# Performance work log

Measured on AMD Instinct MI355X. Metric: run time of the kernel, lower is better.

The kernel has to match this reference:

```python
import jax, jax.numpy as jnp
import numpy as np

B, N, D, H, IN, HID = 16, 1024, 256, 8, 256, 1024
HD = IN // H  # head dim = 32
EPS = 1e-5


def layer_norm(x, g, b):
    mu = jnp.mean(x, axis=-1, keepdims=True)
    var = jnp.var(x, axis=-1, keepdims=True)
    return (x - mu) / jnp.sqrt(var + EPS) * g + b


def setup_inputs() -> dict:
    key = jax.random.key(0)
    ks = jax.random.split(key, 12)
    s = 0.02
    return {
        "x": jax.random.normal(ks[0], (B, N, D), jnp.float32),
        "coords": jax.random.normal(ks[1], (B, N, 2), jnp.float32),
        "g1": jnp.ones((D,), jnp.float32),
        "b1": jnp.zeros((D,), jnp.float32),
        "Wqkv": jax.random.normal(ks[2], (3 * IN, D), jnp.float32) * s,
        "Wproj": jax.random.normal(ks[3], (IN, IN), jnp.float32) * s,
        "bproj": jnp.zeros((IN,), jnp.float32),
        "g2": jnp.ones((D,), jnp.float32),
        "b2": jnp.zeros((D,), jnp.float32),
        "W1": jax.random.normal(ks[4], (HID, D), jnp.float32) * s,
        "bb1": jnp.zeros((HID,), jnp.float32),
        "W2": jax.random.normal(ks[5], (D, HID), jnp.float32) * s,
        "bb2": jnp.zeros((D,), jnp.float32),
    }


def reference(x, coords, g1, b1, Wqkv, Wproj, bproj, g2, b2, W1, bb1, W2, bb2):
    # ---- Attention branch (pre-norm) ----
    h = layer_norm(x, g1, b1)                       # [B,N,D]
    qkv = h @ Wqkv.T                                # [B,N,3*IN]
    qkv = qkv.reshape(B, N, 3, H, HD).transpose(2, 0, 3, 1, 4)  # [3,B,H,N,HD]
    q, k, v = qkv[0], qkv[1], qkv[2]
    scale = HD ** -0.5
    attn = jnp.einsum('bhid,bhjd->bhij', q * scale, k)  # [B,H,N,N]
    attn = jax.nn.softmax(attn, axis=-1)
    o = jnp.einsum('bhij,bhjd->bhid', attn, v)      # [B,H,N,HD]
    o = o.transpose(0, 2, 1, 3).reshape(B, N, IN)   # [B,N,IN]
    o = o @ Wproj.T + bproj
    o = o + h                                       # residual inside Attention (vs normed input)
    x = x + o                                       # Block residual (double residual, faithful)
    # ---- MLP branch ----
    h2 = layer_norm(x, g2, b2)
    m = jax.nn.gelu(h2 @ W1.T + bb1, approximate=False) @ W2.T + bb2
    return x + m
```

## Files before the change

kernel.cpp:

```cpp
#include <hip/hip_runtime.h>
#include <hip/hip_bf16.h>
#include <math.h>

#define Bdim 16
#define Ndim 1024
#define Ddim 256
#define Hdim 8
#define HDdim 32
#define INdim 256
#define HIDdim 1024
#define Tdim (Bdim * Ndim)

typedef __attribute__((ext_vector_type(8)))  short bf16x8;
typedef __attribute__((ext_vector_type(4)))  short bf16x4;
typedef __attribute__((ext_vector_type(16))) float f32x16;
typedef unsigned int u32;

__device__ inline short f2bf(float x) {
    union { __hip_bfloat16 b; short s; } u;
    u.b = __float2bfloat16(x);
    return u.s;
}

__device__ inline float bf2f(short s) {
    return __uint_as_float(((u32)(unsigned short)s) << 16);
}

__device__ inline float fexp2(float x) {
#if __has_builtin(__builtin_amdgcn_exp2f)
    return __builtin_amdgcn_exp2f(x);
#else
    return exp2f(x);
#endif
}

__device__ inline u32 pack2bf(float a, float b) {
#if __has_builtin(__builtin_amdgcn_cvt_pk_bf16_f32)
    typedef __attribute__((ext_vector_type(2))) __bf16 bf16x2_t;
    union { bf16x2_t v; u32 u; } c;
    c.v = __builtin_amdgcn_cvt_pk_bf16_f32(a, b);
    return c.u;
#else
    u32 ua = __float_as_uint(a), ub = __float_as_uint(b);
    return ((ua + 0x8000u) >> 16) | ((ub + 0x8000u) & 0xffff0000u);
#endif
}

__device__ inline void plswap(u32 &a, u32 &b) {
    asm volatile("v_permlane32_swap_b32 %0, %1" : "+v"(a), "+v"(b));
}

__device__ inline float gelu_exact(float v) {
    return 0.5f * v * (1.0f + erff(v * 0.70710678118654752f));
}

#define N4_QKV  (3 * INdim * Ddim / 4)
#define N4_PROJ (INdim * INdim / 4)
#define N4_W1   (HIDdim * Ddim / 4)
#define N4_W2   (Ddim * HIDdim / 4)

__global__ __launch_bounds__(256) void cvt_all_kernel(const float* __restrict__ s0,
                                                      const float* __restrict__ s1,
                                                      const float* __restrict__ s2,
                                                      const float* __restrict__ s3,
                                                      short* __restrict__ d0,
                                                      short* __restrict__ d1,
                                                      short* __restrict__ d2,
                                                      short* __restrict__ d3) {
    int i = blockIdx.x * 256 + threadIdx.x;
    const float* src; short* dst; int j;
    if (i < N4_QKV)                          { src = s0; dst = d0; j = i; }
    else if (i < N4_QKV + N4_PROJ)           { src = s1; dst = d1; j = i - N4_QKV; }
    else if (i < N4_QKV + N4_PROJ + N4_W1)   { src = s2; dst = d2; j = i - N4_QKV - N4_PROJ; }
    else                                     { src = s3; dst = d3; j = i - N4_QKV - N4_PROJ - N4_W1; }
    float4 v = ((const float4*)src)[j];
    bf16x4 b;
    b[0] = f2bf(v.x); b[1] = f2bf(v.y); b[2] = f2bf(v.z); b[3] = f2bf(v.w);
    ((bf16x4*)dst)[j] = b;
}

__global__ __launch_bounds__(256) void ln4_kernel(const float* __restrict__ x,
                                                  const float* __restrict__ g,
                                                  const float* __restrict__ b,
                                                  float* __restrict__ outf,
                                                  short* __restrict__ outb) {
    int w = threadIdx.x >> 6, lane = threadIdx.x & 63;
    int row = blockIdx.x * 4 + w;
    float4 v = ((const float4*)x)[(size_t)row * 64 + lane];
    float s  = (v.x + v.y) + (v.z + v.w);
    float s2 = (v.x * v.x + v.y * v.y) + (v.z * v.z + v.w * v.w);
    #pragma unroll
    for (int off = 32; off; off >>= 1) {
        s  += __shfl_xor(s,  off, 64);
        s2 += __shfl_xor(s2, off, 64);
    }
    float mu   = s * (1.0f / Ddim);
    float var  = s2 * (1.0f / Ddim) - mu * mu;
    float rstd = rsqrtf(var + 1e-5f);
    float4 gg = ((const float4*)g)[lane];
    float4 bb = ((const float4*)b)[lane];
    float4 r;
    r.x = (v.x - mu) * rstd * gg.x + bb.x;
    r.y = (v.y - mu) * rstd * gg.y + bb.y;
    r.z = (v.z - mu) * rstd * gg.z + bb.z;
    r.w = (v.w - mu) * rstd * gg.w + bb.w;
    if (outf) ((float4*)outf)[(size_t)row * 64 + lane] = r;
    bf16x4 rb;
    rb[0] = f2bf(r.x); rb[1] = f2bf(r.y); rb[2] = f2bf(r.z); rb[3] = f2bf(r.w);
    ((bf16x4*)outb)[(size_t)row * 64 + lane] = rb;
}

#define EPI_NONE 0
#define EPI_PROJ 1
#define EPI_GELU 2
#define EPI_RES  3
#define EPI_QKV  4

#define GPAD32 40
#define SCALE2Q 0.25505654249892417f

template <int EPI, int BN>
__global__ __launch_bounds__(256) void gemm_mfma(const short* __restrict__ A,
                                                 const short* __restrict__ W,
                                                 void* __restrict__ Cv,
                                                 int M, int N, int K,
                                                 const float* __restrict__ bias,
                                                 const float* __restrict__ add1,
                                                 const float* __restrict__ add2) {
    __shared__ short As[64 * GPAD32];
    __shared__ short Bs[BN * GPAD32];
    const int tid = threadIdx.x, w = tid >> 6, lane = tid & 63;
    const int col = lane & 31;
    const int half_id = lane >> 5;

    const int nbx = gridDim.x;
    const int flat = blockIdx.y * nbx + blockIdx.x;
    const int cpx = (nbx * (int)gridDim.y) >> 3;
    const int swz = (flat & 7) * cpx + (flat >> 3);
    const int m0 = (swz / nbx) * 64, n0 = (swz % nbx) * BN;

    const int wm = (w & 1) * 32;
    const int wn = (BN == 128) ? (w >> 1) * 64 : (w >> 1) * 32;
    constexpr int TN = (BN == 128) ? 2 : 1;

    f32x16 acc[TN];
    #pragma unroll
    for (int t = 0; t < TN; ++t) acc[t] = 0.0f;

    const int sra = tid >> 2, ssa = (tid & 3) * 8;
    const int srb = (BN == 128) ? (tid >> 1) : (tid >> 2);
    const int ssb = (BN == 128) ? (tid & 1) * 16 : (tid & 3) * 8;
    constexpr int NB = (BN == 128) ? 2 : 1;

    const short* pAsrc = &A[(size_t)(m0 + sra) * K + ssa];
    const short* pBsrc = &W[(size_t)(n0 + srb) * K + ssb];

    bf16x8 pa, pb[NB];
    pa = *(const bf16x8*)&pAsrc[0];
    #pragma unroll
    for (int j = 0; j < NB; ++j) pb[j] = *(const bf16x8*)&pBsrc[j * 8];

    const int T = K >> 5;
    for (int kt = 0; kt < T; ++kt) {
        __syncthreads();
        *(bf16x8*)&As[sra * GPAD32 + ssa] = pa;
        #pragma unroll
        for (int j = 0; j < NB; ++j) *(bf16x8*)&Bs[srb * GPAD32 + ssb + j * 8] = pb[j];
        __syncthreads();

        if (kt + 1 < T) {
            const short* a = pAsrc + (kt + 1) * 32;
            const short* b = pBsrc + (kt + 1) * 32;
            pa = *(const bf16x8*)&a[0];
            #pragma unroll
            for (int j = 0; j < NB; ++j) pb[j] = *(const bf16x8*)&b[j * 8];
        }

        #pragma unroll
        for (int ks = 0; ks < 2; ++ks) {
            bf16x8 af = *(const bf16x8*)&As[(wm + col) * GPAD32 + ks * 16 + half_id * 8];
            bf16x8 bfv[TN];
            #pragma unroll
            for (int t = 0; t < TN; ++t)
                bfv[t] = *(const bf16x8*)&Bs[(wn + t * 32 + col) * GPAD32 + ks * 16 + half_id * 8];
            #pragma unroll
            for (int t = 0; t < TN; ++t)
                acc[t] = __builtin_amdgcn_mfma_f32_32x32x16_bf16(af, bfv[t], acc[t], 0, 0, 0);
        }
    }

    float* Cf = (float*)Cv;
    short* Cb = (short*)Cv;
    #pragma unroll
    for (int r = 0; r < 16; ++r) {
        int row = m0 + wm + (r & 3) + 8 * (r >> 2) + 4 * half_id;
        #pragma unroll
        for (int t = 0; t < TN; ++t) {
            int cn = n0 + wn + t * 32 + col;
            size_t off = (size_t)row * N + cn;
            float v = acc[t][r];
            if (EPI != EPI_NONE && EPI != EPI_QKV) v += bias[cn];
            if (EPI == EPI_QKV && cn < 256) v *= SCALE2Q;
            if (EPI == EPI_GELU) v = gelu_exact(v);
            if (EPI == EPI_PROJ) v += add1[off] + add2[off];
            if (EPI == EPI_RES)  v += add1[off];
            if (EPI == EPI_PROJ || EPI == EPI_RES) Cf[off] = v;
            else                                   Cb[off] = f2bf(v);
        }
    }
}

#define VTPAD 136

__global__ __launch_bounds__(256) void vtrans_kernel(const short* __restrict__ qkv,
                                                     short* __restrict__ vT) {
    __shared__ short Tl[32 * VTPAD];
    const int tid = threadIdx.x;
    const int bh = blockIdx.x, c = blockIdx.y;
    const int b = bh >> 3, head = bh & 7;
    {
        int r = tid >> 1, hv = tid & 1;
        const short* src = qkv + (size_t)b * Ndim * 768 + (size_t)(c * 128 + r) * 768
                           + 512 + head * 32 + hv * 16;
        bf16x8 v0 = *(const bf16x8*)&src[0];
        bf16x8 v1 = *(const bf16x8*)&src[8];
        #pragma unroll
        for (int i = 0; i < 8; ++i) {
            Tl[(hv * 16 + i) * VTPAD + r]     = v0[i];
            Tl[(hv * 16 + 8 + i) * VTPAD + r] = v1[i];
        }
    }
    __syncthreads();
    {
        int d = tid >> 3, j16 = (tid & 7) * 16;
        short* dst = vT + (size_t)(bh * 32 + d) * Ndim + c * 128 + j16;
        *(bf16x8*)&dst[0] = *(const bf16x8*)&Tl[d * VTPAD + j16];
        *(bf16x8*)&dst[8] = *(const bf16x8*)&Tl[d * VTPAD + j16 + 8];
    }
}

#define KVPAD 40
#define CHUNK 128

__global__ __launch_bounds__(256) void attn_mfma_kernel(const short* __restrict__ qkv,
                                                        const short* __restrict__ vT,
                                                        short* __restrict__ opart,
                                                        float* __restrict__ lpart) {
    __shared__ short Ks[CHUNK * KVPAD];
    __shared__ short Vt[32 * VTPAD];

    const int tid = threadIdx.x;
    const int w = tid >> 6;
    const int lane = tid & 63;
    const int col = lane & 31;
    const int half_id = lane >> 5;

    const int bh = blockIdx.y;
    const int b = bh >> 3, head = bh & 7;
    const int q0w = blockIdx.x * 128 + w * 32;
    const int part = blockIdx.z;

    const size_t qkvb = (size_t)b * Ndim * 768;
    short* op = opart + (size_t)part * Tdim * 256;
    float* lp = lpart + (size_t)part * Tdim * 8;

    const int sr = tid >> 1, shv = tid & 1;
    const short* ksrc = qkv + qkvb + (size_t)sr * 768 + 256 + head * 32 + shv * 16;
    const int sd = tid >> 3, sj16 = (tid & 7) * 16;
    const short* vsrc = vT + (size_t)(bh * 32 + sd) * Ndim + sj16;

    bf16x8 qf[2];
    {
        const short* qrow = qkv + qkvb + (size_t)(q0w + col) * 768 + head * 32;
        #pragma unroll
        for (int kh = 0; kh < 2; ++kh)
            qf[kh] = *(const bf16x8*)&qrow[kh * 16 + half_id * 8];
    }

    bf16x8 vone;
    #pragma unroll
    for (int i = 0; i < 8; ++i) vone[i] = (short)0x3F80;

    f32x16 o_acc = 0.0f, l_acc = 0.0f;

    const int c0 = part * 4;

    bf16x8 rk0, rk1, rv0, rv1;
    {
        const short* kp = ksrc + (size_t)(c0 * CHUNK) * 768;
        rk0 = *(const bf16x8*)&kp[0];
        rk1 = *(const bf16x8*)&kp[8];
        const short* vp = vsrc + c0 * CHUNK;
        rv0 = *(const bf16x8*)&vp[0];
        rv1 = *(const bf16x8*)&vp[8];
    }

    #pragma unroll
    for (int ci = 0; ci < 4; ++ci) {
        if (ci != 0) __syncthreads();
        *(bf16x8*)&Ks[sr * KVPAD + shv * 16]     = rk0;
        *(bf16x8*)&Ks[sr * KVPAD + shv * 16 + 8] = rk1;
        *(bf16x8*)&Vt[sd * VTPAD + sj16]     = rv0;
        *(bf16x8*)&Vt[sd * VTPAD + sj16 + 8] = rv1;
        __syncthreads();

        if (ci < 3) {
            const short* kp = ksrc + (size_t)((c0 + ci + 1) * CHUNK) * 768;
            rk0 = *(const bf16x8*)&kp[0];
            rk1 = *(const bf16x8*)&kp[8];
            const short* vp = vsrc + (c0 + ci + 1) * CHUNK;
            rv0 = *(const bf16x8*)&vp[0];
            rv1 = *(const bf16x8*)&vp[8];
        }

        f32x16 s_cur;
        {
            bf16x8 kf0 = *(bf16x8*)&Ks[col * KVPAD + half_id * 8];
            bf16x8 kf1 = *(bf16x8*)&Ks[col * KVPAD + 16 + half_id * 8];
            f32x16 z = 0.0f;
            z = __builtin_amdgcn_mfma_f32_32x32x16_bf16(kf0, qf[0], z, 0, 0, 0);
            z = __builtin_amdgcn_mfma_f32_32x32x16_bf16(kf1, qf[1], z, 0, 0, 0);
            s_cur = z;
        }
        #pragma unroll
        for (int jt = 0; jt < 4; ++jt) {
            f32x16 s_next;
            if (jt < 3) {
                bf16x8 kf0 = *(bf16x8*)&Ks[((jt + 1) * 32 + col) * KVPAD + half_id * 8];
                bf16x8 kf1 = *(bf16x8*)&Ks[((jt + 1) * 32 + col) * KVPAD + 16 + half_id * 8];
                f32x16 z = 0.0f;
                z = __builtin_amdgcn_mfma_f32_32x32x16_bf16(kf0, qf[0], z, 0, 0, 0);
                z = __builtin_amdgcn_mfma_f32_32x32x16_bf16(kf1, qf[1], z, 0, 0, 0);
                s_next = z;
            }

            bf16x8 vf0 = *(bf16x8*)&Vt[col * VTPAD + jt * 32 + half_id * 8];
            bf16x8 vf1 = *(bf16x8*)&Vt[col * VTPAD + jt * 32 + 16 + half_id * 8];

            u32 wd[8];
            #pragma unroll
            for (int g = 0; g < 8; ++g) {
                float e0 = fexp2(s_cur[2 * g + 0]);
                float e1 = fexp2(s_cur[2 * g + 1]);
                wd[g] = pack2bf(e0, e1);
            }
            plswap(wd[0], wd[2]); plswap(wd[1], wd[3]);
            plswap(wd[4], wd[6]); plswap(wd[5], wd[7]);

            union { u32 u[4]; bf16x8 v; } p0, p1;
            p0.u[0] = wd[0]; p0.u[1] = wd[1]; p0.u[2] = wd[2]; p0.u[3] = wd[3];
            p1.u[0] = wd[4]; p1.u[1] = wd[5]; p1.u[2] = wd[6]; p1.u[3] = wd[7];

            __builtin_amdgcn_s_setprio(1);
            o_acc = __builtin_amdgcn_mfma_f32_32x32x16_bf16(p0.v, vf0, o_acc, 0, 0, 0);
            o_acc = __builtin_amdgcn_mfma_f32_32x32x16_bf16(p1.v, vf1, o_acc, 0, 0, 0);
            l_acc = __builtin_amdgcn_mfma_f32_32x32x16_bf16(p0.v, vone, l_acc, 0, 0, 0);
            l_acc = __builtin_amdgcn_mfma_f32_32x32x16_bf16(p1.v, vone, l_acc, 0, 0, 0);
            __builtin_amdgcn_s_setprio(0);

            if (jt < 3) s_cur = s_next;
        }
    }

    #pragma unroll
    for (int r = 0; r < 16; ++r) {
        int q_r = (r & 3) + 8 * (r >> 2) + 4 * half_id;
        size_t gq = (size_t)(b * Ndim + q0w + q_r);
        op[gq * INdim + head * 32 + col] = f2bf(o_acc[r]);
    }
    if (col < 16) {
        int r = col;
        int q_r = (r & 3) + 8 * (r >> 2) + 4 * half_id;
        lp[(size_t)(b * Ndim + q0w + q_r) * 8 + head] = l_acc[r];
    }
}

__global__ __launch_bounds__(256) void combine_kernel(const short* __restrict__ opart,
                                                      const float* __restrict__ lpart,
                                                      short* __restrict__ oat) {
    int i = blockIdx.x * 256 + threadIdx.x;
    size_t base = (size_t)i * 8;
    int gq = (int)(base >> 8);
    int head = ((int)(base & 255)) >> 5;
    bf16x8 a = ((const bf16x8*)opart)[i];
    bf16x8 b = ((const bf16x8*)(opart + (size_t)Tdim * 256))[i];
    float l = lpart[(size_t)gq * 8 + head] + lpart[(size_t)Tdim * 8 + (size_t)gq * 8 + head];
    float rl = 1.0f / l;
    bf16x8 r;
    #pragma unroll
    for (int j = 0; j < 8; ++j) r[j] = f2bf((bf2f(a[j]) + bf2f(b[j])) * rl);
    ((bf16x8*)oat)[i] = r;
}

extern "C" void kernel_launch(void* const* d_in, const int* in_sizes, int n_in,
                              void* d_out, int out_size, void* d_ws, size_t ws_size,
                              hipStream_t stream) {
    const float* x     = (const float*)d_in[0];
    const float* g1    = (const float*)d_in[2];
    const float* b1    = (const float*)d_in[3];
    const float* Wqkv  = (const float*)d_in[4];
    const float* Wproj = (const float*)d_in[5];
    const float* bproj = (const float*)d_in[6];
    const float* g2    = (const float*)d_in[7];
    const float* b2    = (const float*)d_in[8];
    const float* W1    = (const float*)d_in[9];
    const float* bb1   = (const float*)d_in[10];
    const float* W2    = (const float*)d_in[11];
    const float* bb2   = (const float*)d_in[12];
    float* out = (float*)d_out;

    char* ws = (char*)d_ws;
    float* h      = (float*)(ws);
    short* h_bf   = (short*)(ws + (size_t)(16u << 20));
    short* qkv_bf = (short*)(ws + (size_t)(24u << 20));
    float* xnew   = (float*)(ws + (size_t)(24u << 20));
    short* oat_bf = (short*)(ws + (size_t)(40u << 20));
    short* opart  = (short*)(ws + (size_t)(48u << 20));
    short* mid_bf = (short*)(ws + (size_t)(48u << 20));
    float* lpart  = (float*)(ws + (size_t)(80u << 20));
    short* vT     = (short*)(ws + (size_t)(81u << 20));
    short* wqkv_b = (short*)(ws + (size_t)(89u << 20));
    short* wproj_b= (short*)(ws + (size_t)(89u << 20) + 768 * 1024);
    short* w1_b   = (short*)(ws + (size_t)(90u << 20));
    short* w2_b   = (short*)(ws + (size_t)(90u << 20) + 512 * 1024);

    cvt_all_kernel<<<(N4_QKV + N4_PROJ + N4_W1 + N4_W2 + 255) / 256, 256, 0, stream>>>(
        Wqkv, Wproj, W1, W2, wqkv_b, wproj_b, w1_b, w2_b);

    ln4_kernel<<<Tdim / 4, 256, 0, stream>>>(x, g1, b1, h, h_bf);
    gemm_mfma<EPI_QKV, 128><<<dim3(768 / 128, Tdim / 64), 256, 0, stream>>>(
        h_bf, wqkv_b, qkv_bf, Tdim, 768, 256, nullptr, nullptr, nullptr);
    vtrans_kernel<<<dim3(Bdim * Hdim, Ndim / 128), 256, 0, stream>>>(qkv_bf, vT);
    attn_mfma_kernel<<<dim3(Ndim / 128, Bdim * Hdim, 2), 256, 0, stream>>>(
        qkv_bf, vT, opart, lpart);
    combine_kernel<<<(Tdim * INdim / 8) / 256, 256, 0, stream>>>(opart, lpart, oat_bf);
    gemm_mfma<EPI_PROJ, 64><<<dim3(256 / 64, Tdim / 64), 256, 0, stream>>>(
        oat_bf, wproj_b, xnew, Tdim, 256, 256, bproj, h, x);
    ln4_kernel<<<Tdim / 4, 256, 0, stream>>>(xnew, g2, b2, nullptr, h_bf);
    gemm_mfma<EPI_GELU, 128><<<dim3(1024 / 128, Tdim / 64), 256, 0, stream>>>(
        h_bf, w1_b, mid_bf, Tdim, 1024, 256, bb1, nullptr, nullptr);
    gemm_mfma<EPI_RES, 64><<<dim3(256 / 64, Tdim / 64), 256, 0, stream>>>(
        mid_bf, w2_b, out, Tdim, 256, 1024, bb2, xnew, nullptr);
}
```

Baseline: 214.9 us.

## Fuse split-attention combine into proj GEMM and double-buffer GEMM LDS

Removes the standalone combine kernel. The projection GEMM now loads both partial attention outputs and their softmax denominators and normalizes them while staging A tiles into shared memory. All GEMMs also switch to a double-buffered LDS pipeline with two register sets, which halves the barriers per k-step. This saves one kernel launch and one intermediate round trip, at the cost of more registers and LDS and extra A-side loads in the proj GEMM.

```diff
diff --git a/kernel.cpp b/kernel.cpp
--- a/kernel.cpp
+++ b/kernel.cpp
@@ -52,6 +52,12 @@
 
 __device__ inline float gelu_exact(float v) {
     return 0.5f * v * (1.0f + erff(v * 0.70710678118654752f));
+}
+
+__device__ inline void bar_nodrain() {
+    asm volatile("s_waitcnt lgkmcnt(0)" ::: "memory");
+    __builtin_amdgcn_s_barrier();
+    asm volatile("" ::: "memory");
 }
 
 #define N4_QKV  (3 * INdim * Ddim / 4)
@@ -119,16 +125,24 @@
 #define GPAD32 40
 #define SCALE2Q 0.25505654249892417f
 
-template <int EPI, int BN>
+__device__ inline bf16x8 comb8(bf16x8 a, bf16x8 b, float rl) {
+    bf16x8 r;
+    #pragma unroll
+    for (int i = 0; i < 8; ++i) r[i] = f2bf((bf2f(a[i]) + bf2f(b[i])) * rl);
+    return r;
+}
+
+template <int EPI, int BN, bool COMB>
 __global__ __launch_bounds__(256) void gemm_mfma(const short* __restrict__ A,
                                                  const short* __restrict__ W,
                                                  void* __restrict__ Cv,
                                                  int M, int N, int K,
                                                  const float* __restrict__ bias,
                                                  const float* __restrict__ add1,
-                                                 const float* __restrict__ add2) {
-    __shared__ short As[64 * GPAD32];
-    __shared__ short Bs[BN * GPAD32];
+                                                 const float* __restrict__ add2,
+                                                 const float* __restrict__ lpc) {
+    __shared__ short As[2][64 * GPAD32];
+    __shared__ short Bs[2][BN * GPAD32];
     const int tid = threadIdx.x, w = tid >> 6, lane = tid & 63;
     const int col = lane & 31;
     const int half_id = lane >> 5;
@@ -154,39 +168,60 @@
 
     const short* pAsrc = &A[(size_t)(m0 + sra) * K + ssa];
     const short* pBsrc = &W[(size_t)(n0 + srb) * K + ssb];
-
-    bf16x8 pa, pb[NB];
-    pa = *(const bf16x8*)&pAsrc[0];
-    #pragma unroll
-    for (int j = 0; j < NB; ++j) pb[j] = *(const bf16x8*)&pBsrc[j * 8];
-
-    const int T = K >> 5;
-    for (int kt = 0; kt < T; ++kt) {
-        __syncthreads();
-        *(bf16x8*)&As[sra * GPAD32 + ssa] = pa;
-        #pragma unroll
-        for (int j = 0; j < NB; ++j) *(bf16x8*)&Bs[srb * GPAD32 + ssb + j * 8] = pb[j];
-        __syncthreads();
-
-        if (kt + 1 < T) {
-            const short* a = pAsrc + (kt + 1) * 32;
-            const short* b = pBsrc + (kt + 1) * 32;
-            pa = *(const bf16x8*)&a[0];
-            #pragma unroll
-            for (int j = 0; j < NB; ++j) pb[j] = *(const bf16x8*)&b[j * 8];
-        }
-
+    const float* lpr0 = COMB ? (lpc + (size_t)(m0 + sra) * 8) : nullptr;
+    const float* lpr1 = COMB ? (lpr0 + (size_t)Tdim * 8) : nullptr;
+
+    bf16x8 ax, ax2, bx[NB];  float lx = 0.0f;
+    bf16x8 ay, ay2, by[NB];  float ly = 0.0f;
+
+    auto LOADSET = [&](bf16x8& aa, bf16x8& aa2, float& ll, bf16x8* bb, int t) {
+        const short* ap = pAsrc + t * 32;
+        aa = *(const bf16x8*)ap;
+        if constexpr (COMB) {
+            aa2 = *(const bf16x8*)(ap + (size_t)Tdim * 256);
+            ll = lpr0[t] + lpr1[t];
+        }
+        #pragma unroll
+        for (int j = 0; j < NB; ++j) bb[j] = *(const bf16x8*)&pBsrc[t * 32 + j * 8];
+    };
+    auto WRITESET = [&](int buf, bf16x8 aa, bf16x8 aa2, float ll, const bf16x8* bb) {
+        bf16x8 av = aa;
+        if constexpr (COMB) av = comb8(aa, aa2, 1.0f / ll);
+        *(bf16x8*)&As[buf][sra * GPAD32 + ssa] = av;
+        #pragma unroll
+        for (int j = 0; j < NB; ++j) *(bf16x8*)&Bs[buf][srb * GPAD32 + ssb + j * 8] = bb[j];
+    };
+    auto COMPUTEB = [&](int buf) {
         #pragma unroll
         for (int ks = 0; ks < 2; ++ks) {
-            bf16x8 af = *(const bf16x8*)&As[(wm + col) * GPAD32 + ks * 16 + half_id * 8];
+            bf16x8 af = *(const bf16x8*)&As[buf][(wm + col) * GPAD32 + ks * 16 + half_id * 8];
             bf16x8 bfv[TN];
             #pragma unroll
             for (int t = 0; t < TN; ++t)
-                bfv[t] = *(const bf16x8*)&Bs[(wn + t * 32 + col) * GPAD32 + ks * 16 + half_id * 8];
+                bfv[t] = *(const bf16x8*)&Bs[buf][(wn + t * 32 + col) * GPAD32 + ks * 16 + half_id * 8];
             #pragma unroll
             for (int t = 0; t < TN; ++t)
                 acc[t] = __builtin_amdgcn_mfma_f32_32x32x16_bf16(af, bfv[t], acc[t], 0, 0, 0);
         }
+    };
+
+    const int T = K >> 5;
+
+    LOADSET(ax, ax2, lx, bx, 0);
+    LOADSET(ay, ay2, ly, by, 1);
+    WRITESET(0, ax, ax2, lx, bx);
+    LOADSET(ax, ax2, lx, bx, 2);
+    bar_nodrain();
+
+    for (int kt2 = 0; kt2 < T; kt2 += 2) {
+        WRITESET(1, ay, ay2, ly, by);
+        if (kt2 + 3 < T) LOADSET(ay, ay2, ly, by, kt2 + 3);
+        COMPUTEB(0);
+        bar_nodrain();
+        if (kt2 + 2 < T) WRITESET(0, ax, ax2, lx, bx);
+        if (kt2 + 4 < T) LOADSET(ax, ax2, lx, bx, kt2 + 4);
+        COMPUTEB(1);
+        bar_nodrain();
     }
 
     float* Cf = (float*)Cv;
@@ -373,23 +408,6 @@
         int q_r = (r & 3) + 8 * (r >> 2) + 4 * half_id;
         lp[(size_t)(b * Ndim + q0w + q_r) * 8 + head] = l_acc[r];
     }
-}
-
-__global__ __launch_bounds__(256) void combine_kernel(const short* __restrict__ opart,
-                                                      const float* __restrict__ lpart,
-                                                      short* __restrict__ oat) {
-    int i = blockIdx.x * 256 + threadIdx.x;
-    size_t base = (size_t)i * 8;
-    int gq = (int)(base >> 8);
-    int head = ((int)(base & 255)) >> 5;
-    bf16x8 a = ((const bf16x8*)opart)[i];
-    bf16x8 b = ((const bf16x8*)(opart + (size_t)Tdim * 256))[i];
-    float l = lpart[(size_t)gq * 8 + head] + lpart[(size_t)Tdim * 8 + (size_t)gq * 8 + head];
-    float rl = 1.0f / l;
-    bf16x8 r;
-    #pragma unroll
-    for (int j = 0; j < 8; ++j) r[j] = f2bf((bf2f(a[j]) + bf2f(b[j])) * rl);
-    ((bf16x8*)oat)[i] = r;
 }
 
 extern "C" void kernel_launch(void* const* d_in, const int* in_sizes, int n_in,
@@ -414,7 +432,6 @@
     short* h_bf   = (short*)(ws + (size_t)(16u << 20));
     short* qkv_bf = (short*)(ws + (size_t)(24u << 20));
     float* xnew   = (float*)(ws + (size_t)(24u << 20));
-    short* oat_bf = (short*)(ws + (size_t)(40u << 20));
     short* opart  = (short*)(ws + (size_t)(48u << 20));
     short* mid_bf = (short*)(ws + (size_t)(48u << 20));
     float* lpart  = (float*)(ws + (size_t)(80u << 20));
@@ -428,17 +445,16 @@
         Wqkv, Wproj, W1, W2, wqkv_b, wproj_b, w1_b, w2_b);
 
     ln4_kernel<<<Tdim / 4, 256, 0, stream>>>(x, g1, b1, h, h_bf);
-    gemm_mfma<EPI_QKV, 128><<<dim3(768 / 128, Tdim / 64), 256, 0, stream>>>(
-        h_bf, wqkv_b, qkv_bf, Tdim, 768, 256, nullptr, nullptr, nullptr);
+    gemm_mfma<EPI_QKV, 128, false><<<dim3(768 / 128, Tdim / 64), 256, 0, stream>>>(
+        h_bf, wqkv_b, qkv_bf, Tdim, 768, 256, nullptr, nullptr, nullptr, nullptr);
     vtrans_kernel<<<dim3(Bdim * Hdim, Ndim / 128), 256, 0, stream>>>(qkv_bf, vT);
     attn_mfma_kernel<<<dim3(Ndim / 128, Bdim * Hdim, 2), 256, 0, stream>>>(
         qkv_bf, vT, opart, lpart);
-    combine_kernel<<<(Tdim * INdim / 8) / 256, 256, 0, stream>>>(opart, lpart, oat_bf);
-    gemm_mfma<EPI_PROJ, 64><<<dim3(256 / 64, Tdim / 64), 256, 0, stream>>>(
-        oat_bf, wproj_b, xnew, Tdim, 256, 256, bproj, h, x);
+    gemm_mfma<EPI_PROJ, 64, true><<<dim3(256 / 64, Tdim / 64), 256, 0, stream>>>(
+        opart, wproj_b, xnew, Tdim, 256, 256, bproj, h, x, lpart);
     ln4_kernel<<<Tdim / 4, 256, 0, stream>>>(xnew, g2, b2, nullptr, h_bf);
-    gemm_mfma<EPI_GELU, 128><<<dim3(1024 / 128, Tdim / 64), 256, 0, stream>>>(
-        h_bf, w1_b, mid_bf, Tdim, 1024, 256, bb1, nullptr, nullptr);
-    gemm_mfma<EPI_RES, 64><<<dim3(256 / 64, Tdim / 64), 256, 0, stream>>>(
-        mid_bf, w2_b, out, Tdim, 256, 1024, bb2, xnew, nullptr);
-}
+    gemm_mfma<EPI_GELU, 128, false><<<dim3(1024 / 128, Tdim / 64), 256, 0, stream>>>(
+        h_bf, w1_b, mid_bf, Tdim, 1024, 256, bb1, nullptr, nullptr, nullptr);
+    gemm_mfma<EPI_RES, 64, false><<<dim3(256 / 64, Tdim / 64), 256, 0, stream>>>(
+        mid_bf, w2_b, out, Tdim, 256, 1024, bb2, xnew, nullptr, nullptr);
+}
```

New measurement: 216.9 us. Within noise of the previous version (+0.9%).
